# Performance work log

Hardware: AMD Instinct MI355X
Metric: run time of the kernel (lower is better)

The kernel has to match this reference:

```python
import jax, jax.numpy as jnp
import numpy as np

D_IN = 1024
D_OUT = 1024
NUM_HEADS = 16
HEAD_DIM = D_OUT // NUM_HEADS


def setup_inputs() -> dict:
    key = jax.random.key(0)
    k = jax.random.split(key, 6)
    s = 1.0 / np.sqrt(D_IN)
    return {
        "x": jax.random.normal(k[0], (2, 2048, D_IN), dtype=jnp.float32),
        "W_q": jax.random.uniform(k[1], (D_OUT, D_IN), jnp.float32, -s, s),
        "W_k": jax.random.uniform(k[2], (D_OUT, D_IN), jnp.float32, -s, s),
        "W_v": jax.random.uniform(k[3], (D_OUT, D_IN), jnp.float32, -s, s),
        "W_o": jax.random.uniform(k[4], (D_OUT, D_OUT), jnp.float32, -s, s),
        "b_o": jax.random.uniform(k[5], (D_OUT,), jnp.float32, -s, s),
    }


def reference(x, W_q, W_k, W_v, W_o, b_o):
    b, n, _ = x.shape
    h, hd = NUM_HEADS, HEAD_DIM
    # linear projections (torch Linear: x @ W.T), reshape to [b, h, n, hd]
    q = (x @ W_q.T).reshape(b, n, h, hd).transpose(0, 2, 1, 3)
    k = (x @ W_k.T).reshape(b, n, h, hd).transpose(0, 2, 1, 3)
    v = (x @ W_v.T).reshape(b, n, h, hd).transpose(0, 2, 1, 3)
    scores = jnp.einsum("bhqd,bhkd->bhqk", q, k) / np.sqrt(hd).astype(np.float32)
    causal = jnp.triu(jnp.full((n, n), -jnp.inf, dtype=scores.dtype), k=1)
    scores = scores + causal[None, None]
    weights = jax.nn.softmax(scores, axis=-1)  # dropout p=0.0 -> identity
    ctx = jnp.einsum("bhqk,bhkd->bhqd", weights, v)
    ctx = ctx.transpose(0, 2, 1, 3).reshape(b, n, h * hd)
    return ctx @ W_o.T + b_o
```

## Files before the change

### kernel.cpp

```cpp
#include <hip/hip_runtime.h>
#include <hip/hip_bf16.h>
#include <stdint.h>

typedef __attribute__((ext_vector_type(8)))  __bf16   bf16x8;
typedef __attribute__((ext_vector_type(4)))  float    f32x4;
typedef __attribute__((ext_vector_type(16))) float    f32x16;
typedef __attribute__((ext_vector_type(4)))  unsigned u32x4;
typedef __attribute__((ext_vector_type(2)))  unsigned u32x2;

#define BATCH  2
#define SEQ    2048
#define DMODEL 1024
#define NHEAD  16
#define HDIM   64
#define MTOT   (BATCH * SEQ)
#define MOFF   8.0f

__device__ __forceinline__ void gload_lds16(const void* g, void* l) {
  __builtin_amdgcn_global_load_lds(
      (const __attribute__((address_space(1))) unsigned int*)g,
      (__attribute__((address_space(3))) unsigned int*)(uintptr_t)l,
      16, 0, 0);
}

__device__ __forceinline__ unsigned pkbf(float a, float b) {
  unsigned lo = (unsigned)__builtin_bit_cast(unsigned short, (__bf16)a);
  unsigned hb = (unsigned)__builtin_bit_cast(unsigned short, (__bf16)b);
  return lo | (hb << 16);
}

__global__ void cast_all(const float* __restrict__ x,  const float* __restrict__ wq,
                         const float* __restrict__ wk, const float* __restrict__ wv,
                         const float* __restrict__ wo,
                         __bf16* __restrict__ xb,  __bf16* __restrict__ wqb,
                         __bf16* __restrict__ wkb, __bf16* __restrict__ wvb,
                         __bf16* __restrict__ wob)
{
  const float* in; __bf16* out; int n;
  switch (blockIdx.y) {
    case 0:  in = x;  out = xb;  n = MTOT * DMODEL;   break;
    case 1:  in = wq; out = wqb; n = DMODEL * DMODEL; break;
    case 2:  in = wk; out = wkb; n = DMODEL * DMODEL; break;
    case 3:  in = wv; out = wvb; n = DMODEL * DMODEL; break;
    default: in = wo; out = wob; n = DMODEL * DMODEL; break;
  }
  const int i = blockIdx.x * blockDim.x + threadIdx.x;
  const int stride = gridDim.x * blockDim.x;
  for (int idx = i; idx * 8 < n; idx += stride) {
    const float4 a = ((const float4*)in)[idx * 2];
    const float4 b = ((const float4*)in)[idx * 2 + 1];
    bf16x8 v = { (__bf16)a.x, (__bf16)a.y, (__bf16)a.z, (__bf16)a.w,
                 (__bf16)b.x, (__bf16)b.y, (__bf16)b.z, (__bf16)b.w };
    *(bf16x8*)(out + (size_t)idx * 8) = v;
  }
}

__device__ __forceinline__ void gemm_tile_128(const __bf16* __restrict__ A,
                                              const __bf16* __restrict__ W,
                                              int bm, int bn, int Kd,
                                              f32x4 (&acc)[4][4])
{
  __shared__ __align__(16) __bf16 As[128 * 32];
  __shared__ __align__(16) __bf16 Bs[128 * 32];
  const int tid  = threadIdx.x;
  const int wave = tid >> 6, lane = tid & 63;
  const int wr = wave >> 1, wc = wave & 1;
  const int fr = lane & 15, fq = lane >> 4;
  const int c0 = tid, c1 = tid + 256;
  const __bf16* gA0 = A + (size_t)(bm * 128 + (c0 >> 2)) * Kd + (c0 & 3) * 8;
  const __bf16* gA1 = A + (size_t)(bm * 128 + (c1 >> 2)) * Kd + (c1 & 3) * 8;
  const __bf16* gB0 = W + (size_t)(bn * 128 + (c0 >> 2)) * Kd + (c0 & 3) * 8;
  const __bf16* gB1 = W + (size_t)(bn * 128 + (c1 >> 2)) * Kd + (c1 & 3) * 8;

  for (int k0 = 0; k0 < Kd; k0 += 32) {
    gload_lds16(gA0 + k0, As + c0 * 8);
    gload_lds16(gB0 + k0, Bs + c0 * 8);
    gload_lds16(gA1 + k0, As + c1 * 8);
    gload_lds16(gB1 + k0, Bs + c1 * 8);
    __syncthreads();
    bf16x8 a[4], b[4];
#pragma unroll
    for (int m = 0; m < 4; ++m)
      a[m] = *(const bf16x8*)(As + (wr * 64 + m * 16 + fr) * 32 + fq * 8);
#pragma unroll
    for (int n = 0; n < 4; ++n)
      b[n] = *(const bf16x8*)(Bs + (wc * 64 + n * 16 + fr) * 32 + fq * 8);
#pragma unroll
    for (int m = 0; m < 4; ++m)
#pragma unroll
      for (int n = 0; n < 4; ++n)
        acc[m][n] = __builtin_amdgcn_mfma_f32_16x16x32_bf16(a[m], b[n], acc[m][n], 0, 0, 0);
    __syncthreads();
  }
}

__global__ __launch_bounds__(256)
void gemm_qkv(const __bf16* __restrict__ xb,
              const __bf16* __restrict__ Wq, const __bf16* __restrict__ Wk,
              const __bf16* __restrict__ Wv,
              __bf16* __restrict__ Qo, __bf16* __restrict__ Ko, __bf16* __restrict__ VTo,
              float qscale)
{
  const int z = blockIdx.z;
  const __bf16* A; const __bf16* W; __bf16* Ob; int bm, bn;
  if (z == 2)      { A = Wv; W = xb; Ob = VTo; bm = blockIdx.y; bn = blockIdx.x; }
  else if (z == 1) { A = xb; W = Wk; Ob = Ko;  bm = blockIdx.x; bn = blockIdx.y; }
  else             { A = xb; W = Wq; Ob = Qo;  bm = blockIdx.x; bn = blockIdx.y; }

  f32x4 acc[4][4] = {};
  gemm_tile_128(A, W, bm, bn, DMODEL, acc);

  const int lane = threadIdx.x & 63, wave = threadIdx.x >> 6;
  const int wr = wave >> 1, wc = wave & 1;
  const int fr = lane & 15, fq = lane >> 4;

  if (z == 0) {
#pragma unroll
    for (int m = 0; m < 4; ++m)
#pragma unroll
      for (int n = 0; n < 4; ++n) {
        const int col = bn * 128 + wc * 64 + n * 16 + fr;
#pragma unroll
        for (int j = 0; j < 4; ++j) {
          const int row = bm * 128 + wr * 64 + m * 16 + fq * 4 + j;
          Ob[(size_t)row * DMODEL + col] = (__bf16)(acc[m][n][j] * qscale);
        }
      }
  } else if (z == 1) {
#pragma unroll
    for (int m = 0; m < 4; ++m)
#pragma unroll
      for (int n = 0; n < 4; ++n) {
        const int f = bn * 128 + wc * 64 + n * 16 + fr;
        const int h = f >> 6;
        const int kc = (f >> 4) & 3, hi = (f >> 3) & 1, jj = f & 7;
#pragma unroll
        for (int j = 0; j < 4; ++j) {
          const int tkn = bm * 128 + wr * 64 + m * 16 + fq * 4 + j;
          const int bb = tkn >> 11, n2 = tkn & 2047;
          const int t32 = n2 >> 5, ln2 = n2 & 31;
          const size_t idx = (((((size_t)bb * 16 + h) * 64 + t32) * 4 + kc) * 64
                              + (ln2 + (hi << 5))) * 8 + jj;
          Ob[idx] = (__bf16)acc[m][n][j];
        }
      }
  } else {
#pragma unroll
    for (int m = 0; m < 4; ++m)
#pragma unroll
      for (int n = 0; n < 4; ++n) {
        const int tkn = bn * 128 + wc * 64 + n * 16 + fr;
        const int bb = tkn >> 11, n2 = tkn & 2047;
        const int t64 = n2 >> 6, w2 = n2 & 63;
        const int kc = w2 >> 4, hi = (w2 >> 3) & 1, jj = w2 & 7;
#pragma unroll
        for (int j = 0; j < 4; ++j) {
          const int f = bm * 128 + wr * 64 + m * 16 + fq * 4 + j;
          const int h = f >> 6, d = f & 63;
          const int db = d >> 5, ln2 = d & 31;
          const size_t idx = ((((((size_t)bb * 16 + h) * 32 + t64) * 2 + db) * 4 + kc) * 64
                              + (ln2 + (hi << 5))) * 8 + jj;
          Ob[idx] = (__bf16)acc[m][n][j];
        }
      }
  }
}

__global__ __launch_bounds__(256)
void gemm_out(const __bf16* __restrict__ A, const __bf16* __restrict__ W,
              float* __restrict__ OF, const float* __restrict__ bias)
{
  f32x4 acc[4][4] = {};
  gemm_tile_128(A, W, blockIdx.x, blockIdx.y, DMODEL, acc);

  const int lane = threadIdx.x & 63, wave = threadIdx.x >> 6;
  const int wr = wave >> 1, wc = wave & 1;
  const int fr = lane & 15, fq = lane >> 4;
#pragma unroll
  for (int m = 0; m < 4; ++m)
#pragma unroll
    for (int n = 0; n < 4; ++n) {
      const int col = blockIdx.y * 128 + wc * 64 + n * 16 + fr;
#pragma unroll
      for (int j = 0; j < 4; ++j) {
        const int row = blockIdx.x * 128 + wr * 64 + m * 16 + fq * 4 + j;
        OF[(size_t)row * DMODEL + col] = acc[m][n][j] + bias[col];
      }
    }
}


__device__ __forceinline__ void mask_tile(f32x16& sv0, f32x16& sv1,
                                          int kv0, int q0, int ln, int hi)
{
  const int qg = q0 + ln;
#pragma unroll
  for (int r = 0; r < 16; ++r) {
    const int kvo = kv0 + (r & 3) + 8 * (r >> 2) + 4 * hi;
    if (kvo > qg)      sv0[r] = -1e30f;
    if (kvo + 32 > qg) sv1[r] = -1e30f;
  }
}

__device__ __forceinline__ void stream_fin(f32x16& sv0, f32x16& sv1, float& l_acc,
                                           f32x16& c0, f32x16& c1,
                                           const bf16x8 (&vt0)[4], const bf16x8 (&vt1)[4],
                                           int hi)
{
#pragma unroll
  for (int r = 0; r < 16; ++r) {
    sv0[r] = __builtin_amdgcn_exp2f(sv0[r] - MOFF);
    sv1[r] = __builtin_amdgcn_exp2f(sv1[r] - MOFF);
  }
  float s8[8];
#pragma unroll
  for (int r = 0; r < 8; ++r)
    s8[r] = (sv0[r] + sv0[r + 8]) + (sv1[r] + sv1[r + 8]);
#pragma unroll
  for (int r = 0; r < 4; ++r) s8[r] += s8[r + 4];
  l_acc += (s8[0] + s8[1]) + (s8[2] + s8[3]);

  bf16x8 pf[4];
#pragma unroll
  for (int half = 0; half < 2; ++half) {
    const int r0 = half * 8;
    {
      unsigned pk01 = pkbf(sv0[r0 + 0], sv0[r0 + 1]);
      unsigned pk23 = pkbf(sv0[r0 + 2], sv0[r0 + 3]);
      unsigned pk45 = pkbf(sv0[r0 + 4], sv0[r0 + 5]);
      unsigned pk67 = pkbf(sv0[r0 + 6], sv0[r0 + 7]);
      unsigned x01 = (unsigned)__shfl_xor((int)pk01, 32, 64);
      unsigned x23 = (unsigned)__shfl_xor((int)pk23, 32, 64);
      unsigned x45 = (unsigned)__shfl_xor((int)pk45, 32, 64);
      unsigned x67 = (unsigned)__shfl_xor((int)pk67, 32, 64);
      u32x4 uw = { hi ? x45 : pk01, hi ? x67 : pk23,
                   hi ? pk45 : x01, hi ? pk67 : x23 };
      pf[half] = __builtin_bit_cast(bf16x8, uw);
    }
    {
      unsigned pk01 = pkbf(sv1[r0 + 0], sv1[r0 + 1]);
      unsigned pk23 = pkbf(sv1[r0 + 2], sv1[r0 + 3]);
      unsigned pk45 = pkbf(sv1[r0 + 4], sv1[r0 + 5]);
      unsigned pk67 = pkbf(sv1[r0 + 6], sv1[r0 + 7]);
      unsigned x01 = (unsigned)__shfl_xor((int)pk01, 32, 64);
      unsigned x23 = (unsigned)__shfl_xor((int)pk23, 32, 64);
      unsigned x45 = (unsigned)__shfl_xor((int)pk45, 32, 64);
      unsigned x67 = (unsigned)__shfl_xor((int)pk67, 32, 64);
      u32x4 uw = { hi ? x45 : pk01, hi ? x67 : pk23,
                   hi ? pk45 : x01, hi ? pk67 : x23 };
      pf[2 + half] = __builtin_bit_cast(bf16x8, uw);
    }
  }

  __builtin_amdgcn_s_setprio(1);
#pragma unroll
  for (int kc = 0; kc < 4; ++kc)
    c0 = __builtin_amdgcn_mfma_f32_32x32x16_bf16(vt0[kc], pf[kc], c0, 0, 0, 0);
#pragma unroll
  for (int kc = 0; kc < 4; ++kc)
    c1 = __builtin_amdgcn_mfma_f32_32x32x16_bf16(vt1[kc], pf[kc], c1, 0, 0, 0);
  __builtin_amdgcn_s_setprio(0);
}

__global__ __launch_bounds__(128, 2)
void attn_kernel(const __bf16* __restrict__ Qg, const __bf16* __restrict__ PK,
                 const __bf16* __restrict__ PV, __bf16* __restrict__ Og)
{
  __shared__ __align__(16) float Cs[2][32][68];
  __shared__ float Ls[2][2][32];

  const int tid  = threadIdx.x;
  const int p    = tid >> 6;
  const int lane = tid & 63;
  const int ln = lane & 31, hi = lane >> 5;
  const int bI = blockIdx.x;
  const int bh = bI & 31;
  const int jp = bI >> 5;
  const int b = bh >> 4, h = bh & 15;

  const int qtL = jp, qtH = 63 - jp;
  const int q0L = qtL * 32, q0H = qtH * 32;
  const int ntL = (qtL >> 1) + 1, ntH = (qtH >> 1) + 1;

  const __bf16* Kp  = PK + (size_t)(b * 16 + h) * (64 * 4 * 64 * 8);
  const __bf16* Vp  = PV + (size_t)(b * 16 + h) * (32 * 2 * 4 * 64 * 8);
  const __bf16* QpL = Qg + ((size_t)b * SEQ + q0L + ln) * DMODEL + h * HDIM + hi * 8;
  const __bf16* QpH = Qg + ((size_t)b * SEQ + q0H + ln) * DMODEL + h * HDIM + hi * 8;

  bf16x8 qfL[4], qfH[4];
#pragma unroll
  for (int kc = 0; kc < 4; ++kc) {
    qfL[kc] = *(const bf16x8*)(QpL + kc * 16);
    qfH[kc] = *(const bf16x8*)(QpH + kc * 16);
  }

  f32x16 cL0 = {}, cL1 = {}, cH0 = {}, cH1 = {};
  float lL = 0.f, lH = 0.f;

  for (int t = p; t < ntH; t += 2) {
    const __bf16* kt = Kp + (size_t)t * 4096;
    const __bf16* vt = Vp + (size_t)t * 4096;

    bf16x8 kA[4], kB[4], vt0[4], vt1[4];
#pragma unroll
    for (int kc = 0; kc < 4; ++kc) {
      kA[kc]  = *(const bf16x8*)(kt + (kc * 64 + lane) * 8);
      kB[kc]  = *(const bf16x8*)(kt + 2048 + (kc * 64 + lane) * 8);
    }
#pragma unroll
    for (int kc = 0; kc < 4; ++kc) {
      vt0[kc] = *(const bf16x8*)(vt + (kc * 64 + lane) * 8);
      vt1[kc] = *(const bf16x8*)(vt + 2048 + (kc * 64 + lane) * 8);
    }

    const int kv0 = t * 64;

    {
      f32x16 s0 = {}, s1 = {};
      __builtin_amdgcn_s_setprio(1);
#pragma unroll
      for (int kc = 0; kc < 4; ++kc) {
        s0 = __builtin_amdgcn_mfma_f32_32x32x16_bf16(kA[kc], qfH[kc], s0, 0, 0, 0);
        s1 = __builtin_amdgcn_mfma_f32_32x32x16_bf16(kB[kc], qfH[kc], s1, 0, 0, 0);
      }
      __builtin_amdgcn_s_setprio(0);
      if (t == ntH - 1) mask_tile(s0, s1, kv0, q0H, ln, hi);
      stream_fin(s0, s1, lH, cH0, cH1, vt0, vt1, hi);
    }

    if (t < ntL) {
      f32x16 s0 = {}, s1 = {};
      __builtin_amdgcn_s_setprio(1);
#pragma unroll
      for (int kc = 0; kc < 4; ++kc) {
        s0 = __builtin_amdgcn_mfma_f32_32x32x16_bf16(kA[kc], qfL[kc], s0, 0, 0, 0);
        s1 = __builtin_amdgcn_mfma_f32_32x32x16_bf16(kB[kc], qfL[kc], s1, 0, 0, 0);
      }
      __builtin_amdgcn_s_setprio(0);
      if (t == ntL - 1) mask_tile(s0, s1, kv0, q0L, ln, hi);
      stream_fin(s0, s1, lL, cL0, cL1, vt0, vt1, hi);
    }
  }

  if (p == 0) {
#pragma unroll
    for (int g = 0; g < 4; ++g) {
      f32x4 v0 = { cH0[4*g+0], cH0[4*g+1], cH0[4*g+2], cH0[4*g+3] };
      f32x4 v1 = { cH1[4*g+0], cH1[4*g+1], cH1[4*g+2], cH1[4*g+3] };
      *(f32x4*)&Cs[1][ln][g * 8 + hi * 4]      = v0;
      *(f32x4*)&Cs[1][ln][32 + g * 8 + hi * 4] = v1;
    }
    Ls[1][hi][ln] = lH;
  } else {
#pragma unroll
    for (int g = 0; g < 4; ++g) {
      f32x4 v0 = { cL0[4*g+0], cL0[4*g+1], cL0[4*g+2], cL0[4*g+3] };
      f32x4 v1 = { cL1[4*g+0], cL1[4*g+1], cL1[4*g+2], cL1[4*g+3] };
      *(f32x4*)&Cs[0][ln][g * 8 + hi * 4]      = v0;
      *(f32x4*)&Cs[0][ln][32 + g * 8 + hi * 4] = v1;
    }
    Ls[0][hi][ln] = lL;
  }
  __syncthreads();

  if (p == 0) {
    const float lt = lL + __shfl_xor(lL, 32, 64) + Ls[0][0][ln] + Ls[0][1][ln];
    const float inv = 1.0f / lt;
    __bf16* Op = Og + ((size_t)b * SEQ + q0L + ln) * DMODEL + h * HDIM;
#pragma unroll
    for (int g = 0; g < 4; ++g) {
      const f32x4 u0 = *(const f32x4*)&Cs[0][ln][g * 8 + hi * 4];
      const f32x4 u1 = *(const f32x4*)&Cs[0][ln][32 + g * 8 + hi * 4];
      u32x2 w;
      w.x = pkbf((cL0[4*g+0] + u0[0]) * inv, (cL0[4*g+1] + u0[1]) * inv);
      w.y = pkbf((cL0[4*g+2] + u0[2]) * inv, (cL0[4*g+3] + u0[3]) * inv);
      *(u32x2*)(Op + g * 8 + hi * 4) = w;
      w.x = pkbf((cL1[4*g+0] + u1[0]) * inv, (cL1[4*g+1] + u1[1]) * inv);
      w.y = pkbf((cL1[4*g+2] + u1[2]) * inv, (cL1[4*g+3] + u1[3]) * inv);
      *(u32x2*)(Op + 32 + g * 8 + hi * 4) = w;
    }
  } else {
    const float lt = lH + __shfl_xor(lH, 32, 64) + Ls[1][0][ln] + Ls[1][1][ln];
    const float inv = 1.0f / lt;
    __bf16* Op = Og + ((size_t)b * SEQ + q0H + ln) * DMODEL + h * HDIM;
#pragma unroll
    for (int g = 0; g < 4; ++g) {
      const f32x4 u0 = *(const f32x4*)&Cs[1][ln][g * 8 + hi * 4];
      const f32x4 u1 = *(const f32x4*)&Cs[1][ln][32 + g * 8 + hi * 4];
      u32x2 w;
      w.x = pkbf((cH0[4*g+0] + u0[0]) * inv, (cH0[4*g+1] + u0[1]) * inv);
      w.y = pkbf((cH0[4*g+2] + u0[2]) * inv, (cH0[4*g+3] + u0[3]) * inv);
      *(u32x2*)(Op + g * 8 + hi * 4) = w;
      w.x = pkbf((cH1[4*g+0] + u1[0]) * inv, (cH1[4*g+1] + u1[1]) * inv);
      w.y = pkbf((cH1[4*g+2] + u1[2]) * inv, (cH1[4*g+3] + u1[3]) * inv);
      *(u32x2*)(Op + 32 + g * 8 + hi * 4) = w;
    }
  }
}

extern "C" void kernel_launch(void* const* d_in, const int* in_sizes, int n_in,
                              void* d_out, int out_size, void* d_ws, size_t ws_size,
                              hipStream_t stream) {
  (void)in_sizes; (void)n_in; (void)out_size; (void)ws_size;
  const float* x  = (const float*)d_in[0];
  const float* Wq = (const float*)d_in[1];
  const float* Wk = (const float*)d_in[2];
  const float* Wv = (const float*)d_in[3];
  const float* Wo = (const float*)d_in[4];
  const float* bo = (const float*)d_in[5];
  float* out = (float*)d_out;

  __bf16* ws  = (__bf16*)d_ws;
  __bf16* xb  = ws;
  __bf16* Wqb = xb  + (size_t)MTOT * DMODEL;
  __bf16* Wkb = Wqb + (size_t)DMODEL * DMODEL;
  __bf16* Wvb = Wkb + (size_t)DMODEL * DMODEL;
  __bf16* Wob = Wvb + (size_t)DMODEL * DMODEL;
  __bf16* Qb  = Wob + (size_t)DMODEL * DMODEL;
  __bf16* Kpk = Qb  + (size_t)MTOT * DMODEL;
  __bf16* Vpk = Kpk + (size_t)MTOT * DMODEL;
  __bf16* ctxb = xb;

  cast_all<<<dim3(256, 5), 256, 0, stream>>>(x, Wq, Wk, Wv, Wo,
                                             xb, Wqb, Wkb, Wvb, Wob);

  const float qscale = 0.125f * 1.4426950408889634f;
  gemm_qkv<<<dim3(32, 8, 3), 256, 0, stream>>>(xb, Wqb, Wkb, Wvb, Qb, Kpk, Vpk, qscale);

  attn_kernel<<<dim3(1024), 128, 0, stream>>>(Qb, Kpk, Vpk, ctxb);

  gemm_out<<<dim3(32, 8), 256, 0, stream>>>(ctxb, Wob, out, bo);
}
```

Before: 100.1 us.

## Split attention KV loop across four waves with LDS reduction of partial outputs

The attention kernel now runs with 256 threads (4 waves) per block instead of 128, and each wave handles every fourth KV tile rather than every second. Partial context accumulators and row sums from all four waves are reduced through shared memory in two phases (low and high query tile), and the output is written with wider 16-byte stores. This is meant to shorten the serial per-block KV loop and add memory-level parallelism. In exchange it doubles the shared-memory buffers, adds extra barriers and reduction work, and drops the occupancy hint from the launch bounds.

```diff
diff --git a/kernel.cpp b/kernel.cpp
--- a/kernel.cpp
+++ b/kernel.cpp
@@ -262,12 +262,12 @@
   __builtin_amdgcn_s_setprio(0);
 }
 
-__global__ __launch_bounds__(128, 2)
+__global__ __launch_bounds__(256)
 void attn_kernel(const __bf16* __restrict__ Qg, const __bf16* __restrict__ PK,
                  const __bf16* __restrict__ PV, __bf16* __restrict__ Og)
 {
-  __shared__ __align__(16) float Cs[2][32][68];
-  __shared__ float Ls[2][2][32];
+  __shared__ __align__(16) float Cs[4][32][68];
+  __shared__ float Ls[4][2][32];
 
   const int tid  = threadIdx.x;
   const int p    = tid >> 6;
@@ -297,7 +297,7 @@
   f32x16 cL0 = {}, cL1 = {}, cH0 = {}, cH1 = {};
   float lL = 0.f, lH = 0.f;
 
-  for (int t = p; t < ntH; t += 2) {
+  for (int t = p; t < ntH; t += 4) {
     const __bf16* kt = Kp + (size_t)t * 4096;
     const __bf16* vt = Vp + (size_t)t * 4096;
 
@@ -342,59 +342,60 @@
     }
   }
 
-  if (p == 0) {
-#pragma unroll
-    for (int g = 0; g < 4; ++g) {
-      f32x4 v0 = { cH0[4*g+0], cH0[4*g+1], cH0[4*g+2], cH0[4*g+3] };
-      f32x4 v1 = { cH1[4*g+0], cH1[4*g+1], cH1[4*g+2], cH1[4*g+3] };
-      *(f32x4*)&Cs[1][ln][g * 8 + hi * 4]      = v0;
-      *(f32x4*)&Cs[1][ln][32 + g * 8 + hi * 4] = v1;
-    }
-    Ls[1][hi][ln] = lH;
-  } else {
-#pragma unroll
-    for (int g = 0; g < 4; ++g) {
-      f32x4 v0 = { cL0[4*g+0], cL0[4*g+1], cL0[4*g+2], cL0[4*g+3] };
-      f32x4 v1 = { cL1[4*g+0], cL1[4*g+1], cL1[4*g+2], cL1[4*g+3] };
-      *(f32x4*)&Cs[0][ln][g * 8 + hi * 4]      = v0;
-      *(f32x4*)&Cs[0][ln][32 + g * 8 + hi * 4] = v1;
-    }
-    Ls[0][hi][ln] = lL;
-  }
+  const int qe = (p << 3) | (lane >> 3);
+  const int de = (lane & 7) * 8;
+
+#pragma unroll
+  for (int g = 0; g < 4; ++g) {
+    f32x4 v0 = { cL0[4*g+0], cL0[4*g+1], cL0[4*g+2], cL0[4*g+3] };
+    f32x4 v1 = { cL1[4*g+0], cL1[4*g+1], cL1[4*g+2], cL1[4*g+3] };
+    *(f32x4*)&Cs[p][ln][g * 8 + hi * 4]      = v0;
+    *(f32x4*)&Cs[p][ln][32 + g * 8 + hi * 4] = v1;
+  }
+  Ls[p][hi][ln] = lL;
   __syncthreads();
 
-  if (p == 0) {
-    const float lt = lL + __shfl_xor(lL, 32, 64) + Ls[0][0][ln] + Ls[0][1][ln];
+  {
+    float lt = 0.f;
+#pragma unroll
+    for (int pp = 0; pp < 4; ++pp) lt += Ls[pp][0][qe] + Ls[pp][1][qe];
     const float inv = 1.0f / lt;
-    __bf16* Op = Og + ((size_t)b * SEQ + q0L + ln) * DMODEL + h * HDIM;
-#pragma unroll
-    for (int g = 0; g < 4; ++g) {
-      const f32x4 u0 = *(const f32x4*)&Cs[0][ln][g * 8 + hi * 4];
-      const f32x4 u1 = *(const f32x4*)&Cs[0][ln][32 + g * 8 + hi * 4];
-      u32x2 w;
-      w.x = pkbf((cL0[4*g+0] + u0[0]) * inv, (cL0[4*g+1] + u0[1]) * inv);
-      w.y = pkbf((cL0[4*g+2] + u0[2]) * inv, (cL0[4*g+3] + u0[3]) * inv);
-      *(u32x2*)(Op + g * 8 + hi * 4) = w;
-      w.x = pkbf((cL1[4*g+0] + u1[0]) * inv, (cL1[4*g+1] + u1[1]) * inv);
-      w.y = pkbf((cL1[4*g+2] + u1[2]) * inv, (cL1[4*g+3] + u1[3]) * inv);
-      *(u32x2*)(Op + 32 + g * 8 + hi * 4) = w;
-    }
-  } else {
-    const float lt = lH + __shfl_xor(lH, 32, 64) + Ls[1][0][ln] + Ls[1][1][ln];
+    f32x4 a0 = {}, a1 = {};
+#pragma unroll
+    for (int pp = 0; pp < 4; ++pp) {
+      a0 += *(const f32x4*)&Cs[pp][qe][de];
+      a1 += *(const f32x4*)&Cs[pp][qe][de + 4];
+    }
+    u32x4 w = { pkbf(a0[0] * inv, a0[1] * inv), pkbf(a0[2] * inv, a0[3] * inv),
+                pkbf(a1[0] * inv, a1[1] * inv), pkbf(a1[2] * inv, a1[3] * inv) };
+    *(u32x4*)(Og + ((size_t)b * SEQ + q0L + qe) * DMODEL + h * HDIM + de) = w;
+  }
+  __syncthreads();
+
+#pragma unroll
+  for (int g = 0; g < 4; ++g) {
+    f32x4 v0 = { cH0[4*g+0], cH0[4*g+1], cH0[4*g+2], cH0[4*g+3] };
+    f32x4 v1 = { cH1[4*g+0], cH1[4*g+1], cH1[4*g+2], cH1[4*g+3] };
+    *(f32x4*)&Cs[p][ln][g * 8 + hi * 4]      = v0;
+    *(f32x4*)&Cs[p][ln][32 + g * 8 + hi * 4] = v1;
+  }
+  Ls[p][hi][ln] = lH;
+  __syncthreads();
+
+  {
+    float lt = 0.f;
+#pragma unroll
+    for (int pp = 0; pp < 4; ++pp) lt += Ls[pp][0][qe] + Ls[pp][1][qe];
     const float inv = 1.0f / lt;
-    __bf16* Op = Og + ((size_t)b * SEQ + q0H + ln) * DMODEL + h * HDIM;
-#pragma unroll
-    for (int g = 0; g < 4; ++g) {
-      const f32x4 u0 = *(const f32x4*)&Cs[1][ln][g * 8 + hi * 4];
-      const f32x4 u1 = *(const f32x4*)&Cs[1][ln][32 + g * 8 + hi * 4];
-      u32x2 w;
-      w.x = pkbf((cH0[4*g+0] + u0[0]) * inv, (cH0[4*g+1] + u0[1]) * inv);
-      w.y = pkbf((cH0[4*g+2] + u0[2]) * inv, (cH0[4*g+3] + u0[3]) * inv);
-      *(u32x2*)(Op + g * 8 + hi * 4) = w;
-      w.x = pkbf((cH1[4*g+0] + u1[0]) * inv, (cH1[4*g+1] + u1[1]) * inv);
-      w.y = pkbf((cH1[4*g+2] + u1[2]) * inv, (cH1[4*g+3] + u1[3]) * inv);
-      *(u32x2*)(Op + 32 + g * 8 + hi * 4) = w;
-    }
+    f32x4 a0 = {}, a1 = {};
+#pragma unroll
+    for (int pp = 0; pp < 4; ++pp) {
+      a0 += *(const f32x4*)&Cs[pp][qe][de];
+      a1 += *(const f32x4*)&Cs[pp][qe][de + 4];
+    }
+    u32x4 w = { pkbf(a0[0] * inv, a0[1] * inv), pkbf(a0[2] * inv, a0[3] * inv),
+                pkbf(a1[0] * inv, a1[1] * inv), pkbf(a1[2] * inv, a1[3] * inv) };
+    *(u32x4*)(Og + ((size_t)b * SEQ + q0H + qe) * DMODEL + h * HDIM + de) = w;
   }
 }
 
@@ -427,7 +428,7 @@
   const float qscale = 0.125f * 1.4426950408889634f;
   gemm_qkv<<<dim3(32, 8, 3), 256, 0, stream>>>(xb, Wqb, Wkb, Wvb, Qb, Kpk, Vpk, qscale);
 
-  attn_kernel<<<dim3(1024), 128, 0, stream>>>(Qb, Kpk, Vpk, ctxb);
+  attn_kernel<<<dim3(1024), 256, 0, stream>>>(Qb, Kpk, Vpk, ctxb);
 
   gemm_out<<<dim3(32, 8), 256, 0, stream>>>(ctxb, Wob, out, bo);
 }
```

Measured after the change: 121.5 us. 21.4% more time.

## Split attention loop into joint low/high phase and high-only tail

Applied to the files above, without the earlier changes.

Splits the KV-tile loop in two. The first phase covers tiles shared by both query tiles and interleaves their QK MFMAs, exp and PV MFMAs, so the two independent streams expose more ILP and the per-tile `t < ntL` branch goes away. V loads are moved after the QK MFMAs so they overlap with compute. The launch bounds drop the min-2-waves hint, which lets the compiler use more registers for the larger live set at the cost of occupancy.

```diff
diff --git a/kernel.cpp b/kernel.cpp
--- a/kernel.cpp
+++ b/kernel.cpp
@@ -202,25 +202,9 @@
   }
 }
 
-__device__ __forceinline__ void stream_fin(f32x16& sv0, f32x16& sv1, float& l_acc,
-                                           f32x16& c0, f32x16& c1,
-                                           const bf16x8 (&vt0)[4], const bf16x8 (&vt1)[4],
-                                           int hi)
-{
-#pragma unroll
-  for (int r = 0; r < 16; ++r) {
-    sv0[r] = __builtin_amdgcn_exp2f(sv0[r] - MOFF);
-    sv1[r] = __builtin_amdgcn_exp2f(sv1[r] - MOFF);
-  }
-  float s8[8];
-#pragma unroll
-  for (int r = 0; r < 8; ++r)
-    s8[r] = (sv0[r] + sv0[r + 8]) + (sv1[r] + sv1[r + 8]);
-#pragma unroll
-  for (int r = 0; r < 4; ++r) s8[r] += s8[r + 4];
-  l_acc += (s8[0] + s8[1]) + (s8[2] + s8[3]);
-
-  bf16x8 pf[4];
+__device__ __forceinline__ void pack_pf(const f32x16& sv0, const f32x16& sv1,
+                                        bf16x8 (&pf)[4], int hi)
+{
 #pragma unroll
   for (int half = 0; half < 2; ++half) {
     const int r0 = half * 8;
@@ -251,18 +235,9 @@
       pf[2 + half] = __builtin_bit_cast(bf16x8, uw);
     }
   }
-
-  __builtin_amdgcn_s_setprio(1);
-#pragma unroll
-  for (int kc = 0; kc < 4; ++kc)
-    c0 = __builtin_amdgcn_mfma_f32_32x32x16_bf16(vt0[kc], pf[kc], c0, 0, 0, 0);
-#pragma unroll
-  for (int kc = 0; kc < 4; ++kc)
-    c1 = __builtin_amdgcn_mfma_f32_32x32x16_bf16(vt1[kc], pf[kc], c1, 0, 0, 0);
-  __builtin_amdgcn_s_setprio(0);
-}
-
-__global__ __launch_bounds__(128, 2)
+}
+
+__global__ __launch_bounds__(128)
 void attn_kernel(const __bf16* __restrict__ Qg, const __bf16* __restrict__ PK,
                  const __bf16* __restrict__ PV, __bf16* __restrict__ Og)
 {
@@ -297,49 +272,118 @@
   f32x16 cL0 = {}, cL1 = {}, cH0 = {}, cH1 = {};
   float lL = 0.f, lH = 0.f;
 
-  for (int t = p; t < ntH; t += 2) {
+  int t = p;
+
+  for (; t < ntL; t += 2) {
     const __bf16* kt = Kp + (size_t)t * 4096;
     const __bf16* vt = Vp + (size_t)t * 4096;
 
+    bf16x8 kA[4], kB[4];
+#pragma unroll
+    for (int kc = 0; kc < 4; ++kc) {
+      kA[kc] = *(const bf16x8*)(kt + (kc * 64 + lane) * 8);
+      kB[kc] = *(const bf16x8*)(kt + 2048 + (kc * 64 + lane) * 8);
+    }
+
+    f32x16 sH0 = {}, sH1 = {}, sL0 = {}, sL1 = {};
+#pragma unroll
+    for (int kc = 0; kc < 4; ++kc) {
+      sH0 = __builtin_amdgcn_mfma_f32_32x32x16_bf16(kA[kc], qfH[kc], sH0, 0, 0, 0);
+      sL0 = __builtin_amdgcn_mfma_f32_32x32x16_bf16(kA[kc], qfL[kc], sL0, 0, 0, 0);
+      sH1 = __builtin_amdgcn_mfma_f32_32x32x16_bf16(kB[kc], qfH[kc], sH1, 0, 0, 0);
+      sL1 = __builtin_amdgcn_mfma_f32_32x32x16_bf16(kB[kc], qfL[kc], sL1, 0, 0, 0);
+    }
+
+    bf16x8 vt0[4], vt1[4];
+#pragma unroll
+    for (int kc = 0; kc < 4; ++kc) {
+      vt0[kc] = *(const bf16x8*)(vt + (kc * 64 + lane) * 8);
+      vt1[kc] = *(const bf16x8*)(vt + 2048 + (kc * 64 + lane) * 8);
+    }
+
+    if (t == ntL - 1) mask_tile(sL0, sL1, t * 64, q0L, ln, hi);
+
+#pragma unroll
+    for (int r = 0; r < 16; ++r) {
+      sH0[r] = __builtin_amdgcn_exp2f(sH0[r] - MOFF);
+      sL0[r] = __builtin_amdgcn_exp2f(sL0[r] - MOFF);
+      sH1[r] = __builtin_amdgcn_exp2f(sH1[r] - MOFF);
+      sL1[r] = __builtin_amdgcn_exp2f(sL1[r] - MOFF);
+    }
+    float hA[8], lA[8];
+#pragma unroll
+    for (int r = 0; r < 8; ++r) {
+      hA[r] = (sH0[r] + sH0[r + 8]) + (sH1[r] + sH1[r + 8]);
+      lA[r] = (sL0[r] + sL0[r + 8]) + (sL1[r] + sL1[r + 8]);
+    }
+#pragma unroll
+    for (int r = 0; r < 4; ++r) { hA[r] += hA[r + 4]; lA[r] += lA[r + 4]; }
+    lH += (hA[0] + hA[1]) + (hA[2] + hA[3]);
+    lL += (lA[0] + lA[1]) + (lA[2] + lA[3]);
+
+    bf16x8 pfH[4], pfL[4];
+    pack_pf(sH0, sH1, pfH, hi);
+    pack_pf(sL0, sL1, pfL, hi);
+
+#pragma unroll
+    for (int kc = 0; kc < 4; ++kc) {
+      cH0 = __builtin_amdgcn_mfma_f32_32x32x16_bf16(vt0[kc], pfH[kc], cH0, 0, 0, 0);
+      cL0 = __builtin_amdgcn_mfma_f32_32x32x16_bf16(vt0[kc], pfL[kc], cL0, 0, 0, 0);
+    }
+#pragma unroll
+    for (int kc = 0; kc < 4; ++kc) {
+      cH1 = __builtin_amdgcn_mfma_f32_32x32x16_bf16(vt1[kc], pfH[kc], cH1, 0, 0, 0);
+      cL1 = __builtin_amdgcn_mfma_f32_32x32x16_bf16(vt1[kc], pfL[kc], cL1, 0, 0, 0);
+    }
+  }
+
+  for (; t < ntH; t += 2) {
+    const __bf16* kt = Kp + (size_t)t * 4096;
+    const __bf16* vt = Vp + (size_t)t * 4096;
+
     bf16x8 kA[4], kB[4], vt0[4], vt1[4];
 #pragma unroll
     for (int kc = 0; kc < 4; ++kc) {
       kA[kc]  = *(const bf16x8*)(kt + (kc * 64 + lane) * 8);
       kB[kc]  = *(const bf16x8*)(kt + 2048 + (kc * 64 + lane) * 8);
-    }
-#pragma unroll
-    for (int kc = 0; kc < 4; ++kc) {
       vt0[kc] = *(const bf16x8*)(vt + (kc * 64 + lane) * 8);
       vt1[kc] = *(const bf16x8*)(vt + 2048 + (kc * 64 + lane) * 8);
     }
 
-    const int kv0 = t * 64;
-
-    {
-      f32x16 s0 = {}, s1 = {};
-      __builtin_amdgcn_s_setprio(1);
-#pragma unroll
-      for (int kc = 0; kc < 4; ++kc) {
-        s0 = __builtin_amdgcn_mfma_f32_32x32x16_bf16(kA[kc], qfH[kc], s0, 0, 0, 0);
-        s1 = __builtin_amdgcn_mfma_f32_32x32x16_bf16(kB[kc], qfH[kc], s1, 0, 0, 0);
-      }
-      __builtin_amdgcn_s_setprio(0);
-      if (t == ntH - 1) mask_tile(s0, s1, kv0, q0H, ln, hi);
-      stream_fin(s0, s1, lH, cH0, cH1, vt0, vt1, hi);
-    }
-
-    if (t < ntL) {
-      f32x16 s0 = {}, s1 = {};
-      __builtin_amdgcn_s_setprio(1);
-#pragma unroll
-      for (int kc = 0; kc < 4; ++kc) {
-        s0 = __builtin_amdgcn_mfma_f32_32x32x16_bf16(kA[kc], qfL[kc], s0, 0, 0, 0);
-        s1 = __builtin_amdgcn_mfma_f32_32x32x16_bf16(kB[kc], qfL[kc], s1, 0, 0, 0);
-      }
-      __builtin_amdgcn_s_setprio(0);
-      if (t == ntL - 1) mask_tile(s0, s1, kv0, q0L, ln, hi);
-      stream_fin(s0, s1, lL, cL0, cL1, vt0, vt1, hi);
-    }
+    f32x16 s0 = {}, s1 = {};
+    __builtin_amdgcn_s_setprio(1);
+#pragma unroll
+    for (int kc = 0; kc < 4; ++kc) {
+      s0 = __builtin_amdgcn_mfma_f32_32x32x16_bf16(kA[kc], qfH[kc], s0, 0, 0, 0);
+      s1 = __builtin_amdgcn_mfma_f32_32x32x16_bf16(kB[kc], qfH[kc], s1, 0, 0, 0);
+    }
+    __builtin_amdgcn_s_setprio(0);
+    if (t == ntH - 1) mask_tile(s0, s1, t * 64, q0H, ln, hi);
+
+#pragma unroll
+    for (int r = 0; r < 16; ++r) {
+      s0[r] = __builtin_amdgcn_exp2f(s0[r] - MOFF);
+      s1[r] = __builtin_amdgcn_exp2f(s1[r] - MOFF);
+    }
+    float s8[8];
+#pragma unroll
+    for (int r = 0; r < 8; ++r)
+      s8[r] = (s0[r] + s0[r + 8]) + (s1[r] + s1[r + 8]);
+#pragma unroll
+    for (int r = 0; r < 4; ++r) s8[r] += s8[r + 4];
+    lH += (s8[0] + s8[1]) + (s8[2] + s8[3]);
+
+    bf16x8 pf[4];
+    pack_pf(s0, s1, pf, hi);
+
+    __builtin_amdgcn_s_setprio(1);
+#pragma unroll
+    for (int kc = 0; kc < 4; ++kc)
+      cH0 = __builtin_amdgcn_mfma_f32_32x32x16_bf16(vt0[kc], pf[kc], cH0, 0, 0, 0);
+#pragma unroll
+    for (int kc = 0; kc < 4; ++kc)
+      cH1 = __builtin_amdgcn_mfma_f32_32x32x16_bf16(vt1[kc], pf[kc], cH1, 0, 0, 0);
+    __builtin_amdgcn_s_setprio(0);
   }
 
   if (p == 0) {
```

After: 110.8 us. 10.7% more time.
